# Kernel tuning notes

Measured on AMD Instinct MI355X. Metric: run time of the kernel, lower is better.

The kernel has to match this reference:

```python
import jax, jax.numpy as jnp
import numpy as np

B, D, ATT, C = 256, 2048, 512, 1024
TEMP = 4.0  # cfg.JS_Softmax_Temp
SCALE = 20.0
N_GROUPS = 32


def setup_inputs() -> dict:
    key = jax.random.key(0)
    k1, k2, k3, k4 = jax.random.split(key, 4)
    x = jax.random.normal(k1, (B, D), dtype=jnp.float32)
    gt_s_labels = jax.random.randint(k2, (B,), 0, N_GROUPS)
    W = jax.random.normal(k3, (ATT, D), dtype=jnp.float32) * 0.02  # Linear weight [out,in]
    b = jnp.zeros((ATT,), dtype=jnp.float32)
    seen_att = jax.random.normal(k4, (C, ATT), dtype=jnp.float32)
    return {"x": x, "gt_s_labels": gt_s_labels, "W": W, "b": b, "seen_att": seen_att}


def _l2norm(v):
    return v / jnp.maximum(jnp.linalg.norm(v, axis=-1, keepdims=True), 1e-12)


def _adv_loss(x, W, b, seen_att, labels):
    # GRL is identity in forward; classifier = Linear(D, ATT)
    y_att = _l2norm(x @ W.T + b)            # [B, ATT]
    sa = _l2norm(seen_att)                   # [C, ATT]
    logits = SCALE * (y_att @ sa.T)          # [B, C]
    logP = jax.nn.log_softmax(logits / TEMP, axis=-1)
    P = jnp.exp(logP)                        # [B, C] softmax distributions
    # Pairwise mixture log((p_i + p_j)/2): [B, B, C]
    logM = jnp.log((P[:, None, :] + P[None, :, :]) * 0.5)
    negH = jnp.sum(P * logP, axis=-1)        # [B], = -entropy_i
    cross = jnp.einsum('ic,ijc->ij', P, logM)  # sum_c p_i log m_ij
    A = negH[:, None] - cross                # KL(p_i || m_ij), [B, B]
    JS = 0.5 * (A + A.T)                     # m symmetric => JS_ij
    idx = jnp.arange(B)
    mask = (labels[:, None] == labels[None, :]) & (idx[None, :] > idx[:, None])
    cnt = jnp.sum(mask)
    loss = jnp.where(cnt == 0, jnp.float32(0.0),
                     jnp.sum(jnp.where(mask, JS, 0.0)) / jnp.maximum(cnt, 1).astype(jnp.float32))
    return loss * (TEMP ** 2)


def reference(x, gt_s_labels, W, b, seen_att):
    return _adv_loss(x, W, b, seen_att, gt_s_labels)
```

## Files before the change

### kernel.cpp

```cpp
#include <hip/hip_runtime.h>
#include <math.h>

static constexpr int Bn  = 256;
static constexpr int Dd  = 2048;
static constexpr int ATT = 512;
static constexpr int Cc  = 1024;
static constexpr int SK1 = 16;
static constexpr int SK2 = 8;

__device__ __forceinline__ float wave_reduce_sum(float v) {
#pragma unroll
    for (int off = 32; off; off >>= 1) v += __shfl_down(v, off, 64);
    return v;
}
__device__ __forceinline__ float wave_reduce_max(float v) {
#pragma unroll
    for (int off = 32; off; off >>= 1) v = fmaxf(v, __shfl_down(v, off, 64));
    return v;
}
__device__ __forceinline__ float block_reduce_sum(float v) {
    __shared__ float sm_s[4];
    v = wave_reduce_sum(v);
    __syncthreads();
    if ((threadIdx.x & 63) == 0) sm_s[threadIdx.x >> 6] = v;
    __syncthreads();
    return sm_s[0] + sm_s[1] + sm_s[2] + sm_s[3];
}
__device__ __forceinline__ float block_reduce_max(float v) {
    __shared__ float sm_m[4];
    v = wave_reduce_max(v);
    __syncthreads();
    if ((threadIdx.x & 63) == 0) sm_m[threadIdx.x >> 6] = v;
    __syncthreads();
    return fmaxf(fmaxf(sm_m[0], sm_m[1]), fmaxf(sm_m[2], sm_m[3]));
}

static constexpr int BM = 128, BN = 64, BK = 32;
__device__ __forceinline__ void gemm_tile(const float* __restrict__ A,
                                          const float* __restrict__ B,
                                          float* __restrict__ dst, int N, int K,
                                          int row0, int col0, int kbase, int kc,
                                          float (*As)[BM + 4], float (*Bs)[BN + 4]) {
    constexpr int FA = BK / 4;
    constexpr int NA = BM * FA / 256;
    constexpr int NB = BN * FA / 256;
    const int tid = threadIdx.x;
    const int tx = tid & 15, ty = tid >> 4;
    float4 pa[NA], pb[NB];
#pragma unroll
    for (int u = 0; u < NA; ++u) {
        const int t = tid + u * 256, r = t / FA, c4 = (t % FA) * 4;
        pa[u] = *(const float4*)(A + (size_t)(row0 + r) * K + kbase + c4);
    }
#pragma unroll
    for (int u = 0; u < NB; ++u) {
        const int t = tid + u * 256, r = t / FA, c4 = (t % FA) * 4;
        pb[u] = *(const float4*)(B + (size_t)(col0 + r) * K + kbase + c4);
    }
    float acc[8][4] = {};
    for (int k0 = kbase; k0 < kbase + kc; k0 += BK) {
        __syncthreads();
#pragma unroll
        for (int u = 0; u < NA; ++u) {
            const int t = tid + u * 256, r = t / FA, c4 = (t % FA) * 4;
            As[c4 + 0][r] = pa[u].x; As[c4 + 1][r] = pa[u].y;
            As[c4 + 2][r] = pa[u].z; As[c4 + 3][r] = pa[u].w;
        }
#pragma unroll
        for (int u = 0; u < NB; ++u) {
            const int t = tid + u * 256, r = t / FA, c4 = (t % FA) * 4;
            Bs[c4 + 0][r] = pb[u].x; Bs[c4 + 1][r] = pb[u].y;
            Bs[c4 + 2][r] = pb[u].z; Bs[c4 + 3][r] = pb[u].w;
        }
        __syncthreads();
        if (k0 + BK < kbase + kc) {
            const int kn = k0 + BK;
#pragma unroll
            for (int u = 0; u < NA; ++u) {
                const int t = tid + u * 256, r = t / FA, c4 = (t % FA) * 4;
                pa[u] = *(const float4*)(A + (size_t)(row0 + r) * K + kn + c4);
            }
#pragma unroll
            for (int u = 0; u < NB; ++u) {
                const int t = tid + u * 256, r = t / FA, c4 = (t % FA) * 4;
                pb[u] = *(const float4*)(B + (size_t)(col0 + r) * K + kn + c4);
            }
        }
#pragma unroll
        for (int k = 0; k < BK; ++k) {
            const float4 a0 = *(const float4*)&As[k][ty * 8];
            const float4 a1 = *(const float4*)&As[k][ty * 8 + 4];
            const float4 b4 = *(const float4*)&Bs[k][tx * 4];
            const float a[8] = {a0.x, a0.y, a0.z, a0.w, a1.x, a1.y, a1.z, a1.w};
            const float b[4] = {b4.x, b4.y, b4.z, b4.w};
#pragma unroll
            for (int u = 0; u < 8; ++u)
#pragma unroll
                for (int w = 0; w < 4; ++w) acc[u][w] = fmaf(a[u], b[w], acc[u][w]);
        }
    }
#pragma unroll
    for (int u = 0; u < 8; ++u) {
        const int r = row0 + ty * 8 + u;
        *(float4*)(dst + (size_t)r * N + col0 + tx * 4) =
            make_float4(acc[u][0], acc[u][1], acc[u][2], acc[u][3]);
    }
}

__global__ __launch_bounds__(256, 2) void k1_gemm1_sanorm(const float* __restrict__ x,
                                                          const float* __restrict__ W,
                                                          const float* __restrict__ seen,
                                                          float* __restrict__ part,
                                                          float* __restrict__ sa,
                                                          int* __restrict__ doneCnt) {
    __shared__ float As[BK][BM + 4];
    __shared__ float Bs[BK][BN + 4];
    const int bid = blockIdx.x, tid = threadIdx.x;
    if (bid < 256) {
        const int bx = bid & 7, by = (bid >> 3) & 1, bz = bid >> 4;
        gemm_tile(x, W, part + (size_t)bz * Bn * ATT, ATT, Dd,
                  by * BM, bx * BN, bz * (Dd / SK1), Dd / SK1, As, Bs);
    } else {
        if (bid == 256 && tid == 0) *doneCnt = 0;
#pragma unroll
        for (int u = 0; u < 4; ++u) {
            const int r = (bid - 256) * 4 + u, c = tid * 2;
            const float2 v = *(const float2*)(seen + (size_t)r * ATT + c);
            float ss = block_reduce_sum(fmaf(v.x, v.x, v.y * v.y));
            const float sc = 1.0f / fmaxf(sqrtf(ss), 1e-12f);
            *(float2*)(sa + (size_t)r * ATT + c) = make_float2(v.x * sc, v.y * sc);
        }
    }
}

__global__ __launch_bounds__(256) void k2_yanorm(const float* __restrict__ part,
                                                 const float* __restrict__ bias,
                                                 float* __restrict__ ya) {
    const int m = blockIdx.x, c = threadIdx.x * 2;
    float2 s = *(const float2*)(bias + c);
#pragma unroll
    for (int z = 0; z < SK1; ++z) {
        const float2 p = *(const float2*)(part + (size_t)z * Bn * ATT + (size_t)m * ATT + c);
        s.x += p.x; s.y += p.y;
    }
    float ss = block_reduce_sum(fmaf(s.x, s.x, s.y * s.y));
    const float sc = 1.0f / fmaxf(sqrtf(ss), 1e-12f);
    *(float2*)(ya + (size_t)m * ATT + c) = make_float2(s.x * sc, s.y * sc);
}

__global__ __launch_bounds__(256, 2) void k3_gemm2(const float* __restrict__ ya,
                                                   const float* __restrict__ sa,
                                                   float* __restrict__ part) {
    __shared__ float As[BK][BM + 4];
    __shared__ float Bs[BK][BN + 4];
    const int bid = blockIdx.x;
    const int bx = bid & 15, by = (bid >> 4) & 1, bz = bid >> 5;
    gemm_tile(ya, sa, part + (size_t)bz * Bn * Cc, Cc, ATT,
              by * BM, bx * BN, bz * (ATT / SK2), ATT / SK2, As, Bs);
}

__global__ __launch_bounds__(256) void k4_softmax(const float* __restrict__ part,
                                                  float* __restrict__ P,
                                                  float* __restrict__ negH) {
    const int i = blockIdx.x, c = threadIdx.x * 4;
    float4 a = make_float4(0.f, 0.f, 0.f, 0.f);
#pragma unroll
    for (int z = 0; z < SK2; ++z) {
        const float4 p = *(const float4*)(part + (size_t)z * Bn * Cc + (size_t)i * Cc + c);
        a.x += p.x; a.y += p.y; a.z += p.z; a.w += p.w;
    }
    float lv[4] = {a.x * 5.0f, a.y * 5.0f, a.z * 5.0f, a.w * 5.0f};
    float lm = fmaxf(fmaxf(lv[0], lv[1]), fmaxf(lv[2], lv[3]));
    lm = block_reduce_max(lm);
    float se = 0.f;
#pragma unroll
    for (int k = 0; k < 4; ++k) se += __expf(lv[k] - lm);
    se = block_reduce_sum(se);
    const float logZ = __logf(se);
    float nh = 0.f;
    float4 pv;
#pragma unroll
    for (int k = 0; k < 4; ++k) {
        const float lp = lv[k] - lm - logZ;
        const float p = __expf(lp);
        (&pv.x)[k] = p;
        nh = fmaf(p, lp, nh);
    }
    *(float4*)(P + (size_t)i * Cc + c) = pv;
    nh = block_reduce_sum(nh);
    if (threadIdx.x == 0) negH[i] = nh;
}

__global__ __launch_bounds__(256) void k5_pairjs_fin(const float* __restrict__ P,
                                                     const float* __restrict__ negH,
                                                     const int* __restrict__ labels,
                                                     float* __restrict__ pairSum,
                                                     float* __restrict__ pairCnt,
                                                     int* __restrict__ doneCnt,
                                                     float* __restrict__ out) {
    const int i = blockIdx.x, tid = threadIdx.x;
    __shared__ int lbl[Bn];
    __shared__ float nh_s[Bn];
    __shared__ int isLast;
    lbl[tid] = labels[tid];
    nh_s[tid] = negH[tid];
    __syncthreads();
    const int li = lbl[i];
    const float4 pi = *(const float4*)(P + (size_t)i * Cc + tid * 4);
    const float nhi = nh_s[i];

    float tsum = 0.f;
    float nsum = 0.f, cnt = 0.f;
    for (int j = i + 1; j < Bn; ++j) {
        if (lbl[j] != li) continue;
        const float4 pj = *(const float4*)(P + (size_t)j * Cc + tid * 4);
        float t;
        t = pi.x + pj.x; tsum = fmaf(t, __logf(0.5f * t), tsum);
        t = pi.y + pj.y; tsum = fmaf(t, __logf(0.5f * t), tsum);
        t = pi.z + pj.z; tsum = fmaf(t, __logf(0.5f * t), tsum);
        t = pi.w + pj.w; tsum = fmaf(t, __logf(0.5f * t), tsum);
        if (tid == 0) { nsum += nhi + nh_s[j]; cnt += 1.0f; }
    }
    const float s = block_reduce_sum(tsum);
    if (tid == 0) {
        pairSum[i] = 0.5f * (nsum - s);
        pairCnt[i] = cnt;
        __threadfence();
        isLast = (atomicAdd(doneCnt, 1) == Bn - 1);
    }
    __syncthreads();
    if (isLast) {
        __threadfence();
        float fs = block_reduce_sum(pairSum[tid]);
        __syncthreads();
        const float fc = block_reduce_sum(pairCnt[tid]);
        if (tid == 0) out[0] = (fc == 0.0f) ? 0.0f : (fs / fc) * 16.0f;
    }
}

extern "C" void kernel_launch(void* const* d_in, const int* in_sizes, int n_in,
                              void* d_out, int out_size, void* d_ws, size_t ws_size,
                              hipStream_t stream) {
    const float* x      = (const float*)d_in[0];
    const int*   labels = (const int*)d_in[1];
    const float* W      = (const float*)d_in[2];
    const float* bias   = (const float*)d_in[3];
    const float* seen   = (const float*)d_in[4];
    float* out = (float*)d_out;

    char* ws = (char*)d_ws;
    float* part    = (float*)(ws);
    float* sa      = (float*)(ws + (8u << 20));
    float* ya      = (float*)(ws + (10u << 20));
    float* P       = (float*)(ws + (10u << 20) + (512u << 10));
    float* negH    = (float*)(ws + (11u << 20) + (512u << 10));
    float* pairSum = negH + Bn;
    float* pairCnt = pairSum + Bn;
    int*   doneCnt = (int*)(pairCnt + Bn);

    k1_gemm1_sanorm<<<512, 256, 0, stream>>>(x, W, seen, part, sa, doneCnt);
    k2_yanorm<<<Bn, 256, 0, stream>>>(part, bias, ya);
    k3_gemm2<<<256, 256, 0, stream>>>(ya, sa, part);
    k4_softmax<<<Bn, 256, 0, stream>>>(part, P, negH);
    k5_pairjs_fin<<<Bn, 256, 0, stream>>>(P, negH, labels, pairSum, pairCnt, doneCnt, out);
}
```

Before: 59.22 us.

## Replace FP32 FMA GEMM tiles with split-bf16 MFMA (3-term hi/lo) emulation

Both GEMMs now split each fp32 operand into a bf16 high part and a bf16 residual, stage them in shared memory in row-major layout, and accumulate hi*hi + hi*lo + lo*hi with 16x16x32 bf16 MFMA instructions. This moves the GEMM work from scalar FMAs onto the matrix cores while keeping close to fp32 accuracy. The cost is extra conversion work and doubled shared-memory traffic during staging, plus scalar (uncoalesced-ish) output stores, and a small precision loss from dropping the lo*lo term.

```diff
diff --git a/kernel.cpp b/kernel.cpp
--- a/kernel.cpp
+++ b/kernel.cpp
@@ -7,6 +7,11 @@
 static constexpr int Cc  = 1024;
 static constexpr int SK1 = 16;
 static constexpr int SK2 = 8;
+static constexpr int BM = 128, BN = 64, BK = 32;
+static constexpr int APITCH = BK + 8;
+
+typedef __attribute__((ext_vector_type(8))) short short8v;
+typedef __attribute__((ext_vector_type(4))) float f32x4;
 
 __device__ __forceinline__ float wave_reduce_sum(float v) {
 #pragma unroll
@@ -35,17 +40,36 @@
     return fmaxf(fmaxf(sm_m[0], sm_m[1]), fmaxf(sm_m[2], sm_m[3]));
 }
 
-static constexpr int BM = 128, BN = 64, BK = 32;
-__device__ __forceinline__ void gemm_tile(const float* __restrict__ A,
-                                          const float* __restrict__ B,
-                                          float* __restrict__ dst, int N, int K,
-                                          int row0, int col0, int kbase, int kc,
-                                          float (*As)[BM + 4], float (*Bs)[BN + 4]) {
+__device__ __forceinline__ void splitbf(float v, unsigned short& h, unsigned short& l) {
+    const unsigned int b = __float_as_uint(v);
+    h = (unsigned short)(b >> 16);
+    const float r = v - __uint_as_float(b & 0xFFFF0000u);
+    l = (unsigned short)(__float_as_uint(r) >> 16);
+}
+__device__ __forceinline__ void stage4(const float4 v, unsigned short* hi,
+                                       unsigned short* lo, int off) {
+    unsigned short h0, h1, h2, h3, l0, l1, l2, l3;
+    splitbf(v.x, h0, l0); splitbf(v.y, h1, l1);
+    splitbf(v.z, h2, l2); splitbf(v.w, h3, l3);
+    *(ushort4*)(hi + off) = make_ushort4(h0, h1, h2, h3);
+    *(ushort4*)(lo + off) = make_ushort4(l0, l1, l2, l3);
+}
+
+__device__ __forceinline__ void gemm_tile_mfma(const float* __restrict__ A,
+                                               const float* __restrict__ B,
+                                               float* __restrict__ dst, int N, int K,
+                                               int row0, int col0, int kbase, int kc,
+                                               unsigned short* __restrict__ Ahi,
+                                               unsigned short* __restrict__ Alo,
+                                               unsigned short* __restrict__ Bhi,
+                                               unsigned short* __restrict__ Blo) {
     constexpr int FA = BK / 4;
     constexpr int NA = BM * FA / 256;
     constexpr int NB = BN * FA / 256;
     const int tid = threadIdx.x;
-    const int tx = tid & 15, ty = tid >> 4;
+    const int lane = tid & 63, wv = tid >> 6;
+    const int fr = lane & 15, fg = lane >> 4;
+
     float4 pa[NA], pb[NB];
 #pragma unroll
     for (int u = 0; u < NA; ++u) {
@@ -57,20 +81,18 @@
         const int t = tid + u * 256, r = t / FA, c4 = (t % FA) * 4;
         pb[u] = *(const float4*)(B + (size_t)(col0 + r) * K + kbase + c4);
     }
-    float acc[8][4] = {};
+    f32x4 acc[2][4] = {};
     for (int k0 = kbase; k0 < kbase + kc; k0 += BK) {
         __syncthreads();
 #pragma unroll
         for (int u = 0; u < NA; ++u) {
             const int t = tid + u * 256, r = t / FA, c4 = (t % FA) * 4;
-            As[c4 + 0][r] = pa[u].x; As[c4 + 1][r] = pa[u].y;
-            As[c4 + 2][r] = pa[u].z; As[c4 + 3][r] = pa[u].w;
+            stage4(pa[u], Ahi, Alo, r * APITCH + c4);
         }
 #pragma unroll
         for (int u = 0; u < NB; ++u) {
             const int t = tid + u * 256, r = t / FA, c4 = (t % FA) * 4;
-            Bs[c4 + 0][r] = pb[u].x; Bs[c4 + 1][r] = pb[u].y;
-            Bs[c4 + 2][r] = pb[u].z; Bs[c4 + 3][r] = pb[u].w;
+            stage4(pb[u], Bhi, Blo, r * APITCH + c4);
         }
         __syncthreads();
         if (k0 + BK < kbase + kc) {
@@ -86,24 +108,37 @@
                 pb[u] = *(const float4*)(B + (size_t)(col0 + r) * K + kn + c4);
             }
         }
-#pragma unroll
-        for (int k = 0; k < BK; ++k) {
-            const float4 a0 = *(const float4*)&As[k][ty * 8];
-            const float4 a1 = *(const float4*)&As[k][ty * 8 + 4];
-            const float4 b4 = *(const float4*)&Bs[k][tx * 4];
-            const float a[8] = {a0.x, a0.y, a0.z, a0.w, a1.x, a1.y, a1.z, a1.w};
-            const float b[4] = {b4.x, b4.y, b4.z, b4.w};
-#pragma unroll
-            for (int u = 0; u < 8; ++u)
-#pragma unroll
-                for (int w = 0; w < 4; ++w) acc[u][w] = fmaf(a[u], b[w], acc[u][w]);
-        }
-    }
-#pragma unroll
-    for (int u = 0; u < 8; ++u) {
-        const int r = row0 + ty * 8 + u;
-        *(float4*)(dst + (size_t)r * N + col0 + tx * 4) =
-            make_float4(acc[u][0], acc[u][1], acc[u][2], acc[u][3]);
+        short8v ah[2], al[2];
+#pragma unroll
+        for (int im = 0; im < 2; ++im) {
+            const int mrow = (wv * 2 + im) * 16 + fr;
+            ah[im] = *(short8v*)(Ahi + mrow * APITCH + fg * 8);
+            al[im] = *(short8v*)(Alo + mrow * APITCH + fg * 8);
+        }
+#pragma unroll
+        for (int in = 0; in < 4; ++in) {
+            const int nrow = in * 16 + fr;
+            const short8v bh = *(short8v*)(Bhi + nrow * APITCH + fg * 8);
+            const short8v bl = *(short8v*)(Blo + nrow * APITCH + fg * 8);
+#pragma unroll
+            for (int im = 0; im < 2; ++im) {
+                acc[im][in] = __builtin_amdgcn_mfma_f32_16x16x32_bf16(ah[im], bh, acc[im][in], 0, 0, 0);
+                acc[im][in] = __builtin_amdgcn_mfma_f32_16x16x32_bf16(ah[im], bl, acc[im][in], 0, 0, 0);
+                acc[im][in] = __builtin_amdgcn_mfma_f32_16x16x32_bf16(al[im], bh, acc[im][in], 0, 0, 0);
+            }
+        }
+    }
+#pragma unroll
+    for (int im = 0; im < 2; ++im) {
+#pragma unroll
+        for (int in = 0; in < 4; ++in) {
+#pragma unroll
+            for (int r = 0; r < 4; ++r) {
+                const int m = row0 + (wv * 2 + im) * 16 + fg * 4 + r;
+                const int c = col0 + in * 16 + fr;
+                dst[(size_t)m * N + c] = acc[im][in][r];
+            }
+        }
     }
 }
 
@@ -113,13 +148,16 @@
                                                           float* __restrict__ part,
                                                           float* __restrict__ sa,
                                                           int* __restrict__ doneCnt) {
-    __shared__ float As[BK][BM + 4];
-    __shared__ float Bs[BK][BN + 4];
+    __shared__ unsigned short AhiS[BM * APITCH];
+    __shared__ unsigned short AloS[BM * APITCH];
+    __shared__ unsigned short BhiS[BN * APITCH];
+    __shared__ unsigned short BloS[BN * APITCH];
     const int bid = blockIdx.x, tid = threadIdx.x;
     if (bid < 256) {
         const int bx = bid & 7, by = (bid >> 3) & 1, bz = bid >> 4;
-        gemm_tile(x, W, part + (size_t)bz * Bn * ATT, ATT, Dd,
-                  by * BM, bx * BN, bz * (Dd / SK1), Dd / SK1, As, Bs);
+        gemm_tile_mfma(x, W, part + (size_t)bz * Bn * ATT, ATT, Dd,
+                       by * BM, bx * BN, bz * (Dd / SK1), Dd / SK1,
+                       AhiS, AloS, BhiS, BloS);
     } else {
         if (bid == 256 && tid == 0) *doneCnt = 0;
 #pragma unroll
@@ -151,12 +189,15 @@
 __global__ __launch_bounds__(256, 2) void k3_gemm2(const float* __restrict__ ya,
                                                    const float* __restrict__ sa,
                                                    float* __restrict__ part) {
-    __shared__ float As[BK][BM + 4];
-    __shared__ float Bs[BK][BN + 4];
+    __shared__ unsigned short AhiS[BM * APITCH];
+    __shared__ unsigned short AloS[BM * APITCH];
+    __shared__ unsigned short BhiS[BN * APITCH];
+    __shared__ unsigned short BloS[BN * APITCH];
     const int bid = blockIdx.x;
     const int bx = bid & 15, by = (bid >> 4) & 1, bz = bid >> 5;
-    gemm_tile(ya, sa, part + (size_t)bz * Bn * Cc, Cc, ATT,
-              by * BM, bx * BN, bz * (ATT / SK2), ATT / SK2, As, Bs);
+    gemm_tile_mfma(ya, sa, part + (size_t)bz * Bn * Cc, Cc, ATT,
+                   by * BM, bx * BN, bz * (ATT / SK2), ATT / SK2,
+                   AhiS, AloS, BhiS, BloS);
 }
 
 __global__ __launch_bounds__(256) void k4_softmax(const float* __restrict__ part,
```

New measurement: 51.39 us. 13.2% less time.
